# Performance work log

Measured on AMD Instinct MI355X. Metric: run time of the kernel, lower is better.

## Reference

```python
import jax, jax.numpy as jnp
import numpy as np

N_NODES = 100000
N_EDGES = 600000
D_NODE = 128
D_EDGE = 128
D_HID = 512
D_OUT = 128


def setup_inputs() -> dict:
    key = jax.random.key(0)
    ks = jax.random.split(key, 8)
    node_features = jax.random.normal(ks[0], (N_NODES, D_NODE), dtype=jnp.float32)
    edge_features = jax.random.normal(ks[1], (N_EDGES, D_EDGE), dtype=jnp.float32)
    src_indices = jax.random.randint(ks[2], (N_EDGES,), 0, N_NODES, dtype=jnp.int64)
    d_in = D_NODE + D_EDGE
    W1 = jax.random.normal(ks[3], (d_in, D_HID), dtype=jnp.float32) / np.sqrt(d_in)
    b1 = jnp.zeros((D_HID,), dtype=jnp.float32)
    W2 = jax.random.normal(ks[4], (D_HID, D_OUT), dtype=jnp.float32) / np.sqrt(D_HID)
    b2 = jnp.zeros((D_OUT,), dtype=jnp.float32)
    ln_gamma = jnp.ones((D_OUT,), dtype=jnp.float32)
    ln_beta = jnp.zeros((D_OUT,), dtype=jnp.float32)
    return {
        "node_features": node_features,
        "edge_features": edge_features,
        "W1": W1, "b1": b1, "W2": W2, "b2": b2,
        "ln_gamma": ln_gamma, "ln_beta": ln_beta,
        "src_indices": src_indices,
    }


def _layer_norm(x, gamma, beta, eps=1e-5):
    mu = jnp.mean(x, axis=-1, keepdims=True)
    var = jnp.var(x, axis=-1, keepdims=True)
    return (x - mu) * jax.lax.rsqrt(var + eps) * gamma + beta


def reference(node_features, edge_features, W1, b1, W2, b2, ln_gamma, ln_beta, src_indices):
    # scatter-sum edges -> nodes  [N, D_EDGE]
    agg = jax.ops.segment_sum(edge_features, src_indices, num_segments=node_features.shape[0])
    x = jnp.concatenate([node_features, agg], axis=-1)  # [N, D_NODE+D_EDGE]
    h = jax.nn.silu(x @ W1 + b1)                         # [N, D_HID]
    y = h @ W2 + b2                                      # [N, D_OUT]
    y = _layer_norm(y, ln_gamma, ln_beta)
    return y + node_features
```

## Files before the change

kernel.cpp:

```cpp
#include <hip/hip_runtime.h>
#include <hip/hip_bf16.h>

namespace {

constexpr int N_NODES = 100000;
constexpr int N_EDGES = 600000;
constexpr int D_NODE  = 128;
constexpr int D_HID   = 512;
constexpr int D_OUT   = 128;

constexpr int CAP = 32;

constexpr int BM = 64;
constexpr int GEMM_GRID = (N_NODES + BM - 1) / BM;

typedef short bf16x8 __attribute__((ext_vector_type(8)));
typedef short bf16x4 __attribute__((ext_vector_type(4)));
typedef float f32x4  __attribute__((ext_vector_type(4)));

__device__ inline ushort f2bf(float x) {
  __hip_bfloat16 b = __float2bfloat16(x);
  return *reinterpret_cast<ushort*>(&b);
}
__device__ inline unsigned pk2(float a, float b) {
  float2 f; f.x = a; f.y = b;
  __hip_bfloat162 p = __float22bfloat162_rn(f);
  return *reinterpret_cast<unsigned*>(&p);
}

__global__ __launch_bounds__(256) void pack_w_kernel(
    const float* __restrict__ W1, const float* __restrict__ W2,
    ushort* __restrict__ W1p, ushort* __restrict__ W2p,
    unsigned* __restrict__ XbPad, int* __restrict__ cnt) {
  const int gid = blockIdx.x * 256 + threadIdx.x;
  if (gid < N_NODES) cnt[gid] = 0;
  if (gid < 4096) XbPad[gid] = 0;
  if (gid < 16384) {
    const int l = gid & 63;
    const int kt = (gid >> 6) & 7;
    const int ntg = gid >> 9;
    const int n = ntg * 16 + (l & 15);
    const int k0 = kt * 32 + (l >> 4) * 8;
    ushort tmp[8];
#pragma unroll
    for (int j = 0; j < 8; ++j) tmp[j] = f2bf(W1[(size_t)(k0 + j) * D_HID + n]);
    *reinterpret_cast<uint4*>(W1p + (size_t)gid * 8) = *reinterpret_cast<uint4*>(tmp);
  } else if (gid < 24576) {
    const int g2 = gid - 16384;
    const int l = g2 & 63;
    const int kt = (g2 >> 6) & 15;
    const int ntg = g2 >> 10;
    const int n = ntg * 16 + (l & 15);
    const int k0 = kt * 32 + (l >> 4) * 8;
    ushort tmp[8];
#pragma unroll
    for (int j = 0; j < 8; ++j) tmp[j] = f2bf(W2[(size_t)(k0 + j) * D_OUT + n]);
    *reinterpret_cast<uint4*>(W2p + (size_t)g2 * 8) = *reinterpret_cast<uint4*>(tmp);
  }
}

__global__ __launch_bounds__(256) void bucket_fill_kernel(
    const int* __restrict__ src, int* __restrict__ cnt, int* __restrict__ elist) {
  const int e = blockIdx.x * blockDim.x + threadIdx.x;
  if (e < N_EDGES) {
    const int s = src[e];
    const int pos = atomicAdd(&cnt[s], 1);
    if (pos < CAP) elist[s * CAP + pos] = e;
  }
}

__global__ __launch_bounds__(256) void gather_kernel(
    const float* __restrict__ nodef, const float* __restrict__ ef,
    const int* __restrict__ cnt, const int* __restrict__ elist,
    unsigned* __restrict__ Xb) {
  const int t = threadIdx.x;
  const int w = t >> 6, l = t & 63;
  const int node = blockIdx.x * 4 + w;
  const int half = l >> 5, lc = l & 31;
  const int deg = min(cnt[node], CAP);
  const int eidx = elist[node * CAP + lc];
  if (half) {
    const float4 nf = *reinterpret_cast<const float4*>(
        nodef + (size_t)node * D_NODE + 4 * lc);
    uint2 u; u.x = pk2(nf.x, nf.y); u.y = pk2(nf.z, nf.w);
    *reinterpret_cast<uint2*>(Xb + (size_t)node * 128 + 2 * lc) = u;
  }
  float a0 = 0.f, a1 = 0.f, a2 = 0.f, a3 = 0.f;
  for (int k = half; k < deg; k += 2) {
    const int e = __shfl(eidx, k);
    const float4 v = *reinterpret_cast<const float4*>(
        ef + (size_t)e * D_NODE + 4 * lc);
    a0 += v.x; a1 += v.y; a2 += v.z; a3 += v.w;
  }
  a0 += __shfl_xor(a0, 32);
  a1 += __shfl_xor(a1, 32);
  a2 += __shfl_xor(a2, 32);
  a3 += __shfl_xor(a3, 32);
  if (!half) {
    uint2 u; u.x = pk2(a0, a1); u.y = pk2(a2, a3);
    *reinterpret_cast<uint2*>(Xb + (size_t)node * 128 + 64 + 2 * lc) = u;
  }
}


#define TR_ISSUE(kt, t0, t1)                                                        \
  {                                                                                 \
    const unsigned base_ = lds0 + (unsigned)(kt) * 1024u;                           \
    asm volatile("ds_read_b64_tr_b16 %0, %1" : "=v"(t0[0]) : "v"(base_));           \
    asm volatile("ds_read_b64_tr_b16 %0, %1 offset:512" : "=v"(t1[0]) : "v"(base_)); \
    asm volatile("ds_read_b64_tr_b16 %0, %1 offset:16384" : "=v"(t0[1]) : "v"(base_)); \
    asm volatile("ds_read_b64_tr_b16 %0, %1 offset:16896" : "=v"(t1[1]) : "v"(base_)); \
    asm volatile("ds_read_b64_tr_b16 %0, %1 offset:32768" : "=v"(t0[2]) : "v"(base_)); \
    asm volatile("ds_read_b64_tr_b16 %0, %1 offset:33280" : "=v"(t1[2]) : "v"(base_)); \
    asm volatile("ds_read_b64_tr_b16 %0, %1 offset:49152" : "=v"(t0[3]) : "v"(base_)); \
    asm volatile("ds_read_b64_tr_b16 %0, %1 offset:49664" : "=v"(t1[3]) : "v"(base_)); \
  }

#define TR_MFMA(t0, t1, bw)                                                         \
  {                                                                                 \
    _Pragma("unroll")                                                               \
    for (int mt_ = 0; mt_ < 4; ++mt_) {                                             \
      const bf16x8 am_ =                                                            \
          __builtin_shufflevector(t0[mt_], t1[mt_], 0, 1, 2, 3, 4, 5, 6, 7);        \
      acc2[mt_] = __builtin_amdgcn_mfma_f32_16x16x32_bf16(am_, bw, acc2[mt_], 0, 0, 0); \
    }                                                                               \
  }

#define LOADW2(kt)                                                                  \
  (*reinterpret_cast<const bf16x8*>(W2p + (size_t)((w * 16 + (kt)) * 64 + l) * 8))

__global__ __launch_bounds__(512, 4) void gemm_kernel(
    const ushort* __restrict__ Xb,
    const ushort* __restrict__ W1p,
    const ushort* __restrict__ W2p,
    const float* __restrict__ b1,
    const float* __restrict__ b2,
    const float* __restrict__ gamma,
    const float* __restrict__ beta,
    float* __restrict__ out) {
  __shared__ ushort Hs[32768];
  __shared__ float mu_s[64], rs_s[64];
  float* Ys = reinterpret_cast<float*>(Hs);

  const int t = threadIdx.x;
  const int w = t >> 6;
  const int l = t & 63;
  const int G = l >> 4;
  const int ln = l & 15;
  const int node0 = blockIdx.x * BM;

  f32x4 acc[4][4];
#pragma unroll
  for (int nt = 0; nt < 4; ++nt) {
    const float bb = b1[w * 64 + nt * 16 + ln];
#pragma unroll
    for (int mt = 0; mt < 4; ++mt) acc[mt][nt] = f32x4{bb, bb, bb, bb};
  }
  const ushort* xr0 = Xb + (size_t)(node0 + ln) * 256;
#pragma unroll 2
  for (int kt = 0; kt < 8; ++kt) {
    bf16x8 a[4];
#pragma unroll
    for (int mt = 0; mt < 4; ++mt)
      a[mt] = *reinterpret_cast<const bf16x8*>(xr0 + mt * 16 * 256 + kt * 32 + G * 8);
#pragma unroll
    for (int nt = 0; nt < 4; ++nt) {
      const bf16x8 b = *reinterpret_cast<const bf16x8*>(
          W1p + (size_t)(((w * 4 + nt) * 8 + kt) * 64 + l) * 8);
#pragma unroll
      for (int mt = 0; mt < 4; ++mt)
        acc[mt][nt] = __builtin_amdgcn_mfma_f32_16x16x32_bf16(a[mt], b, acc[mt][nt], 0, 0, 0);
    }
  }

#pragma unroll
  for (int mt = 0; mt < 4; ++mt) {
#pragma unroll
    for (int nt = 0; nt < 4; ++nt) {
      f32x4 v = acc[mt][nt];
      v.x = v.x / (1.f + __expf(-v.x));
      v.y = v.y / (1.f + __expf(-v.y));
      v.z = v.z / (1.f + __expf(-v.z));
      v.w = v.w / (1.f + __expf(-v.w));
      const int k = w * 64 + nt * 16 + ln;
      const unsigned S = (unsigned)(G * 4 + (k & 3) * 16 + ((k >> 3) & 3) * 64 +
                                    ((k >> 2) & 1) * 256 + (k >> 5) * 512 + mt * 8192);
      uint2 u;
      u.x = pk2(v.x, v.y);
      u.y = pk2(v.z, v.w);
      *reinterpret_cast<uint2*>(&Hs[S]) = u;
    }
  }
  __syncthreads();

  f32x4 acc2[4];
  {
    const float bb = b2[w * 16 + ln];
#pragma unroll
    for (int mt = 0; mt < 4; ++mt) acc2[mt] = f32x4{bb, bb, bb, bb};
  }
  const unsigned lds0 = (unsigned)(size_t)(&Hs[0]) + 8u * (unsigned)l;
  bf16x4 A0[4], A1[4], B0[4], B1[4];
  bf16x8 bwA = LOADW2(0);
  TR_ISSUE(0, A0, A1);
#pragma unroll
  for (int kp = 0; kp < 8; ++kp) {
    const int k1 = 2 * kp + 1;
    const bf16x8 bwB = LOADW2(k1);
    TR_ISSUE(k1, B0, B1);
    asm volatile("s_waitcnt lgkmcnt(8)" ::: "memory");
    __builtin_amdgcn_sched_barrier(0);
    TR_MFMA(A0, A1, bwA);
    if (kp < 7) {
      bwA = LOADW2(k1 + 1);
      TR_ISSUE(k1 + 1, A0, A1);
      asm volatile("s_waitcnt lgkmcnt(8)" ::: "memory");
    } else {
      asm volatile("s_waitcnt lgkmcnt(0)" ::: "memory");
    }
    __builtin_amdgcn_sched_barrier(0);
    TR_MFMA(B0, B1, bwB);
  }
  __syncthreads();

#pragma unroll
  for (int mt = 0; mt < 4; ++mt)
#pragma unroll
    for (int r = 0; r < 4; ++r)
      Ys[(mt * 16 + G * 4 + r) * 132 + (w * 16 + ln)] = acc2[mt][r];
  __syncthreads();
  {
    const int r = t >> 3, k2 = t & 7;
    float s = 0.f, s2 = 0.f;
#pragma unroll
    for (int u = 0; u < 16; ++u) {
      const float v = Ys[r * 132 + k2 + u * 8];
      s += v; s2 += v * v;
    }
#pragma unroll
    for (int off = 1; off < 8; off <<= 1) {
      s  += __shfl_xor(s, off);
      s2 += __shfl_xor(s2, off);
    }
    if (k2 == 0) {
      const float mu  = s * (1.f / 128.f);
      const float var = s2 * (1.f / 128.f) - mu * mu;
      mu_s[r] = mu;
      rs_s[r] = rsqrtf(var + 1e-5f);
    }
  }
  __syncthreads();
  {
    const int c = t & 127, g2 = t >> 7;
    const float gm = gamma[c], bt = beta[c];
#pragma unroll
    for (int m = 0; m < 16; ++m) {
      const int r = g2 * 16 + m;
      const int n = node0 + r;
      if (n < N_NODES) {
        const float nf = __uint_as_float(((unsigned)Xb[(size_t)n * 256 + c]) << 16);
        out[(size_t)n * D_OUT + c] = (Ys[r * 132 + c] - mu_s[r]) * rs_s[r] * gm + bt + nf;
      }
    }
  }
}

}

extern "C" void kernel_launch(void* const* d_in, const int* in_sizes, int n_in,
                              void* d_out, int out_size, void* d_ws, size_t ws_size,
                              hipStream_t stream) {
  const float* nodef = (const float*)d_in[0];
  const float* ef    = (const float*)d_in[1];
  const float* W1    = (const float*)d_in[2];
  const float* b1    = (const float*)d_in[3];
  const float* W2    = (const float*)d_in[4];
  const float* b2    = (const float*)d_in[5];
  const float* gamma = (const float*)d_in[6];
  const float* beta  = (const float*)d_in[7];
  const int*   src   = (const int*)d_in[8];
  float* out = (float*)d_out;

  char* ws = (char*)d_ws;
  ushort* Xb    = (ushort*)ws;
  ushort* W1p   = (ushort*)(ws + 51216384);
  ushort* W2p   = (ushort*)(ws + 51478528);
  int*    cnt   = (int*)   (ws + 51609600);
  int*    elist = (int*)   (ws + 52009600);
  unsigned* XbPad = (unsigned*)(Xb) + (size_t)N_NODES * 128;

  pack_w_kernel<<<391, 256, 0, stream>>>(W1, W2, W1p, W2p, XbPad, cnt);

  const int eblocks = (N_EDGES + 255) / 256;
  bucket_fill_kernel<<<eblocks, 256, 0, stream>>>(src, cnt, elist);

  gather_kernel<<<N_NODES / 4, 256, 0, stream>>>(nodef, ef, cnt, elist,
                                                 (unsigned*)Xb);

  gemm_kernel<<<GEMM_GRID, 512, 0, stream>>>(Xb, W1p, W2p, b1, b2, gamma,
                                             beta, out);
}
```

Baseline: 237.7 us.

## Fuse edge gather and concat into GEMM kernel via swizzled LDS tile

Removes the separate gather kernel and the bf16 X intermediate in global memory. Each GEMM block now gathers its own 64 nodes' features and aggregated edge features into a swizzled LDS tile, then reads the A operand from LDS. It also unrolls the edge accumulation by four to keep more loads in flight. The cost is that the irregular gather latency now sits inside the GEMM kernel, which has limited occupancy, and an extra barrier is added before the hidden tile reuses LDS.

Result: faster. 196.4 us (median of 2 runs) (-17.4%).

```diff
diff --git a/kernel.cpp b/kernel.cpp
--- a/kernel.cpp
+++ b/kernel.cpp
@@ -31,10 +31,9 @@
 __global__ __launch_bounds__(256) void pack_w_kernel(
     const float* __restrict__ W1, const float* __restrict__ W2,
     ushort* __restrict__ W1p, ushort* __restrict__ W2p,
-    unsigned* __restrict__ XbPad, int* __restrict__ cnt) {
+    int* __restrict__ cnt) {
   const int gid = blockIdx.x * 256 + threadIdx.x;
   if (gid < N_NODES) cnt[gid] = 0;
-  if (gid < 4096) XbPad[gid] = 0;
   if (gid < 16384) {
     const int l = gid & 63;
     const int kt = (gid >> 6) & 7;
@@ -66,39 +65,6 @@
     const int s = src[e];
     const int pos = atomicAdd(&cnt[s], 1);
     if (pos < CAP) elist[s * CAP + pos] = e;
-  }
-}
-
-__global__ __launch_bounds__(256) void gather_kernel(
-    const float* __restrict__ nodef, const float* __restrict__ ef,
-    const int* __restrict__ cnt, const int* __restrict__ elist,
-    unsigned* __restrict__ Xb) {
-  const int t = threadIdx.x;
-  const int w = t >> 6, l = t & 63;
-  const int node = blockIdx.x * 4 + w;
-  const int half = l >> 5, lc = l & 31;
-  const int deg = min(cnt[node], CAP);
-  const int eidx = elist[node * CAP + lc];
-  if (half) {
-    const float4 nf = *reinterpret_cast<const float4*>(
-        nodef + (size_t)node * D_NODE + 4 * lc);
-    uint2 u; u.x = pk2(nf.x, nf.y); u.y = pk2(nf.z, nf.w);
-    *reinterpret_cast<uint2*>(Xb + (size_t)node * 128 + 2 * lc) = u;
-  }
-  float a0 = 0.f, a1 = 0.f, a2 = 0.f, a3 = 0.f;
-  for (int k = half; k < deg; k += 2) {
-    const int e = __shfl(eidx, k);
-    const float4 v = *reinterpret_cast<const float4*>(
-        ef + (size_t)e * D_NODE + 4 * lc);
-    a0 += v.x; a1 += v.y; a2 += v.z; a3 += v.w;
-  }
-  a0 += __shfl_xor(a0, 32);
-  a1 += __shfl_xor(a1, 32);
-  a2 += __shfl_xor(a2, 32);
-  a3 += __shfl_xor(a3, 32);
-  if (!half) {
-    uint2 u; u.x = pk2(a0, a1); u.y = pk2(a2, a3);
-    *reinterpret_cast<uint2*>(Xb + (size_t)node * 128 + 64 + 2 * lc) = u;
   }
 }
 
@@ -130,7 +96,10 @@
   (*reinterpret_cast<const bf16x8*>(W2p + (size_t)((w * 16 + (kt)) * 64 + l) * 8))
 
 __global__ __launch_bounds__(512, 4) void gemm_kernel(
-    const ushort* __restrict__ Xb,
+    const float* __restrict__ nodef,
+    const float* __restrict__ ef,
+    const int* __restrict__ cnt,
+    const int* __restrict__ elist,
     const ushort* __restrict__ W1p,
     const ushort* __restrict__ W2p,
     const float* __restrict__ b1,
@@ -141,6 +110,7 @@
   __shared__ ushort Hs[32768];
   __shared__ float mu_s[64], rs_s[64];
   float* Ys = reinterpret_cast<float*>(Hs);
+  char* XsB = reinterpret_cast<char*>(Hs);
 
   const int t = threadIdx.x;
   const int w = t >> 6;
@@ -149,6 +119,52 @@
   const int ln = l & 15;
   const int node0 = blockIdx.x * BM;
 
+  {
+    const int h = l >> 5, lc = l & 31;
+#pragma unroll 1
+    for (int p = 0; p < 4; ++p) {
+      const int r = w * 8 + p * 2 + h;
+      const int node = node0 + r;
+      float4 nf = float4{0.f, 0.f, 0.f, 0.f};
+      float a0 = 0.f, a1 = 0.f, a2 = 0.f, a3 = 0.f;
+      int deg = 0, eidx = 0;
+      if (node < N_NODES) {
+        deg = min(cnt[node], CAP);
+        eidx = elist[node * CAP + lc];
+        nf = *reinterpret_cast<const float4*>(nodef + (size_t)node * D_NODE + 4 * lc);
+      }
+      int k = 0;
+#pragma unroll 1
+      for (; k + 4 <= deg; k += 4) {
+        const int e0 = __shfl(eidx, k + 0, 32);
+        const int e1 = __shfl(eidx, k + 1, 32);
+        const int e2 = __shfl(eidx, k + 2, 32);
+        const int e3 = __shfl(eidx, k + 3, 32);
+        const float4 v0 = *reinterpret_cast<const float4*>(ef + (size_t)e0 * D_NODE + 4 * lc);
+        const float4 v1 = *reinterpret_cast<const float4*>(ef + (size_t)e1 * D_NODE + 4 * lc);
+        const float4 v2 = *reinterpret_cast<const float4*>(ef + (size_t)e2 * D_NODE + 4 * lc);
+        const float4 v3 = *reinterpret_cast<const float4*>(ef + (size_t)e3 * D_NODE + 4 * lc);
+        a0 += (v0.x + v1.x) + (v2.x + v3.x);
+        a1 += (v0.y + v1.y) + (v2.y + v3.y);
+        a2 += (v0.z + v1.z) + (v2.z + v3.z);
+        a3 += (v0.w + v1.w) + (v2.w + v3.w);
+      }
+#pragma unroll 1
+      for (; k < deg; ++k) {
+        const int e = __shfl(eidx, k, 32);
+        const float4 v = *reinterpret_cast<const float4*>(ef + (size_t)e * D_NODE + 4 * lc);
+        a0 += v.x; a1 += v.y; a2 += v.z; a3 += v.w;
+      }
+      const unsigned sw = ((unsigned)(r & 7)) << 4;
+      const unsigned rowbase = (unsigned)r * 512u;
+      uint2 un; un.x = pk2(nf.x, nf.y); un.y = pk2(nf.z, nf.w);
+      *reinterpret_cast<uint2*>(XsB + rowbase + (((unsigned)(lc * 8)) ^ sw)) = un;
+      uint2 ua; ua.x = pk2(a0, a1); ua.y = pk2(a2, a3);
+      *reinterpret_cast<uint2*>(XsB + rowbase + (((unsigned)(256 + lc * 8)) ^ sw)) = ua;
+    }
+  }
+  __syncthreads();
+
   f32x4 acc[4][4];
 #pragma unroll
   for (int nt = 0; nt < 4; ++nt) {
@@ -156,13 +172,16 @@
 #pragma unroll
     for (int mt = 0; mt < 4; ++mt) acc[mt][nt] = f32x4{bb, bb, bb, bb};
   }
-  const ushort* xr0 = Xb + (size_t)(node0 + ln) * 256;
 #pragma unroll 2
   for (int kt = 0; kt < 8; ++kt) {
     bf16x8 a[4];
 #pragma unroll
-    for (int mt = 0; mt < 4; ++mt)
-      a[mt] = *reinterpret_cast<const bf16x8*>(xr0 + mt * 16 * 256 + kt * 32 + G * 8);
+    for (int mt = 0; mt < 4; ++mt) {
+      const int row = mt * 16 + ln;
+      const unsigned boff = (unsigned)row * 512u +
+          (((unsigned)(kt * 64 + G * 16)) ^ (((unsigned)(row & 7)) << 4));
+      a[mt] = *reinterpret_cast<const bf16x8*>(XsB + boff);
+    }
 #pragma unroll
     for (int nt = 0; nt < 4; ++nt) {
       const bf16x8 b = *reinterpret_cast<const bf16x8*>(
@@ -172,6 +191,7 @@
         acc[mt][nt] = __builtin_amdgcn_mfma_f32_16x16x32_bf16(a[mt], b, acc[mt][nt], 0, 0, 0);
     }
   }
+  __syncthreads();
 
 #pragma unroll
   for (int mt = 0; mt < 4; ++mt) {
@@ -258,8 +278,8 @@
       const int r = g2 * 16 + m;
       const int n = node0 + r;
       if (n < N_NODES) {
-        const float nf = __uint_as_float(((unsigned)Xb[(size_t)n * 256 + c]) << 16);
-        out[(size_t)n * D_OUT + c] = (Ys[r * 132 + c] - mu_s[r]) * rs_s[r] * gm + bt + nf;
+        out[(size_t)n * D_OUT + c] = (Ys[r * 132 + c] - mu_s[r]) * rs_s[r] * gm + bt +
+                                     nodef[(size_t)n * D_NODE + c];
       }
     }
   }
@@ -282,21 +302,16 @@
   float* out = (float*)d_out;
 
   char* ws = (char*)d_ws;
-  ushort* Xb    = (ushort*)ws;
-  ushort* W1p   = (ushort*)(ws + 51216384);
-  ushort* W2p   = (ushort*)(ws + 51478528);
-  int*    cnt   = (int*)   (ws + 51609600);
-  int*    elist = (int*)   (ws + 52009600);
-  unsigned* XbPad = (unsigned*)(Xb) + (size_t)N_NODES * 128;
-
-  pack_w_kernel<<<391, 256, 0, stream>>>(W1, W2, W1p, W2p, XbPad, cnt);
+  ushort* W1p   = (ushort*)ws;
+  ushort* W2p   = (ushort*)(ws + 262144);
+  int*    cnt   = (int*)   (ws + 393216);
+  int*    elist = (int*)   (ws + 793216);
+
+  pack_w_kernel<<<391, 256, 0, stream>>>(W1, W2, W1p, W2p, cnt);
 
   const int eblocks = (N_EDGES + 255) / 256;
   bucket_fill_kernel<<<eblocks, 256, 0, stream>>>(src, cnt, elist);
 
-  gather_kernel<<<N_NODES / 4, 256, 0, stream>>>(nodef, ef, cnt, elist,
-                                                 (unsigned*)Xb);
-
-  gemm_kernel<<<GEMM_GRID, 512, 0, stream>>>(Xb, W1p, W2p, b1, b2, gamma,
-                                             beta, out);
-}
+  gemm_kernel<<<GEMM_GRID, 512, 0, stream>>>(nodef, ef, cnt, elist, W1p, W2p,
+                                             b1, b2, gamma, beta, out);
+}
```
